# Performance work log

Hardware: AMD Instinct MI355X
Metric: run time of the kernel (lower is better)

Reference implementation:

```python
import jax, jax.numpy as jnp
import numpy as np

VOC = 50257
EMB = 128
N_MEM = 8192
T_Q = 50
T_M = 50
N_HOPS = 3


def setup_inputs() -> dict:
    key = jax.random.key(0)
    ks = jax.random.split(key, 12)
    s = 0.1
    return {
        "query": jax.random.randint(ks[0], (1, T_Q), 0, VOC, dtype=jnp.int32),
        "story": jax.random.randint(ks[1], (N_MEM, T_M), 0, VOC, dtype=jnp.int32),
        "Wa": s * jax.random.normal(ks[2], (VOC, EMB), dtype=jnp.float32),
        "Wc": s * jax.random.normal(ks[3], (VOC, EMB), dtype=jnp.float32),
        "Wb": s * jax.random.normal(ks[4], (VOC, EMB), dtype=jnp.float32),
        "Wt_w": s * jax.random.normal(ks[5], (EMB, EMB), dtype=jnp.float32),
        "Wt_b": jnp.zeros((EMB,), dtype=jnp.float32),
        "H_w": s * jax.random.normal(ks[6], (EMB, EMB), dtype=jnp.float32),
        "H_b": jnp.zeros((EMB,), dtype=jnp.float32),
        "weight_out": s * jax.random.normal(ks[7], (VOC, EMB), dtype=jnp.float32),
        "TA": s * jax.random.normal(ks[8], (N_MEM, EMB), dtype=jnp.float32),
        "TC": s * jax.random.normal(ks[9], (N_MEM, EMB), dtype=jnp.float32),
    }


def reference(query, story, Wa, Wc, Wb, Wt_w, Wt_b, H_w, H_b, weight_out, TA, TC):
    # compute_weights is a stub in the source -> uniform weights 1.0 (plain sum over tokens)
    u = Wb[query].sum(axis=1)                      # [1, E]
    # layer_wise=True: Wa/Wc/Wt shared across hops, so memories are hop-invariant;
    # gather once (same math as recomputing per hop).
    memory_in = Wa[story].sum(axis=1) + TA         # [N, E]
    memory_out = Wc[story].sum(axis=1) + TC        # [N, E]
    for _ in range(N_HOPS):
        attn = jax.nn.softmax(u @ memory_in.T, axis=-1)   # [1, N]
        weighted_out = attn @ memory_out                  # [1, E]
        t = jax.nn.sigmoid(u @ Wt_w.T + Wt_b)             # [1, E]
        u = u * (1.0 - t) + (weighted_out @ H_w.T + H_b) * t
    return jax.nn.log_softmax(u @ weight_out.T, axis=-1)  # [1, V]
```

## Files before the change

kernel.cpp:

```cpp
#include <hip/hip_runtime.h>

#define VOC 50257
#define EMB 128
#define NMEM 8192
#define TQ 50
#define TM 50
#define NHOPS 3

#define MEM_ROWS 4
#define NMEMBLK (NMEM / MEM_ROWS)
#define NHOP 512
#define HROWS (NMEM / NHOP)
#define LOGROWS 64
#define NLOG ((VOC + LOGROWS - 1) / LOGROWS)

#define WS_U      0
#define WS_MIN    (WS_U + EMB)
#define WS_MOUT   (WS_MIN + NMEM*EMB)
#define WS_BSUM   (WS_MOUT + NMEM*EMB)
#define WS_WPART  (WS_BSUM + NHOP)
#define WS_LOGITS (WS_WPART + NHOP*EMB)
#define WS_BPART  (WS_LOGITS + VOC)

__global__ void k_mem_u(const int* __restrict__ story, const int* __restrict__ query,
                        const float* __restrict__ Wa, const float* __restrict__ Wc,
                        const float* __restrict__ Wb, const float* __restrict__ TA,
                        const float* __restrict__ TC, float* __restrict__ min_,
                        float* __restrict__ mout, float* __restrict__ u) {
    int b = blockIdx.x;
    int t = threadIdx.x;
    if (b == NMEMBLK) {
        __shared__ int q[TQ];
        if (t < TQ) q[t] = query[t];
        __syncthreads();
        if (t < EMB) {
            float acc = 0.f;
            for (int i = 0; i < TQ; ++i) acc += Wb[q[i] * EMB + t];
            u[t] = acc;
        }
        return;
    }
    __shared__ int toks[MEM_ROWS * TM];
    if (t < MEM_ROWS * TM) toks[t] = story[b * MEM_ROWS * TM + t];
    __syncthreads();
    int w = t >> 6;
    int lane = t & 63;
    int half = lane >> 5;
    int l = lane & 31;
    int n = b * MEM_ROWS + w;
    float4 a = {0.f, 0.f, 0.f, 0.f};
    float4 c = {0.f, 0.f, 0.f, 0.f};
    #pragma unroll
    for (int tt = 0; tt < TM / 2; ++tt) {
        int tok = toks[w * TM + 2 * tt + half];
        float4 va = ((const float4*)(Wa + tok * EMB))[l];
        float4 vc = ((const float4*)(Wc + tok * EMB))[l];
        a.x += va.x; a.y += va.y; a.z += va.z; a.w += va.w;
        c.x += vc.x; c.y += vc.y; c.z += vc.z; c.w += vc.w;
    }
    a.x += __shfl_xor(a.x, 32); a.y += __shfl_xor(a.y, 32);
    a.z += __shfl_xor(a.z, 32); a.w += __shfl_xor(a.w, 32);
    c.x += __shfl_xor(c.x, 32); c.y += __shfl_xor(c.y, 32);
    c.z += __shfl_xor(c.z, 32); c.w += __shfl_xor(c.w, 32);
    if (half == 0) {
        float4 tv = ((const float4*)(TA + n * EMB))[l];
        a.x += tv.x; a.y += tv.y; a.z += tv.z; a.w += tv.w;
        ((float4*)(min_ + n * EMB))[l] = a;
    } else {
        float4 tv = ((const float4*)(TC + n * EMB))[l];
        c.x += tv.x; c.y += tv.y; c.z += tv.z; c.w += tv.w;
        ((float4*)(mout + n * EMB))[l] = c;
    }
}

__global__ void k_hop(const float* __restrict__ min_, const float* __restrict__ mout,
                      const float* __restrict__ u, float* __restrict__ bsum,
                      float* __restrict__ wpart) {
    int b = blockIdx.x, t = threadIdx.x;
    int w = t >> 6, l = t & 63;
    __shared__ float2 su[64];
    __shared__ float wgt[HROWS];
    __shared__ float part[EMB];
    if (t < 64) su[t] = ((const float2*)u)[t];
    __syncthreads();
    float2 uv = su[l];
    #pragma unroll
    for (int r = 0; r < HROWS / 4; ++r) {
        int rl = w * (HROWS / 4) + r;
        int n = b * HROWS + rl;
        float2 m = ((const float2*)(min_ + n * EMB))[l];
        float p = uv.x * m.x + uv.y * m.y;
        #pragma unroll
        for (int o = 32; o > 0; o >>= 1) p += __shfl_xor(p, o);
        if (l == 0) wgt[rl] = __expf(p);
    }
    __syncthreads();
    if (t < HROWS) {
        float s = wgt[t];
        #pragma unroll
        for (int o = HROWS / 2; o > 0; o >>= 1) s += __shfl_xor(s, o);
        if (t == 0) bsum[b] = s;
    }
    int c = t & 127, h = t >> 7;
    float acc = 0.f;
    #pragma unroll
    for (int r = 0; r < HROWS / 2; ++r) {
        int rl = h * (HROWS / 2) + r;
        acc += wgt[rl] * mout[(b * HROWS + rl) * EMB + c];
    }
    if (h == 0) part[c] = acc;
    __syncthreads();
    if (h == 1) wpart[b * EMB + c] = part[c] + acc;
}

__global__ void k_upd(const float* __restrict__ bsum, const float* __restrict__ wpart,
                      const float* __restrict__ Wt_w, const float* __restrict__ Wt_b,
                      const float* __restrict__ H_w, const float* __restrict__ H_b,
                      float* __restrict__ u) {
    int t = threadIdx.x;
    __shared__ float red[1024];
    __shared__ float wop[8][EMB];
    __shared__ float tga[8][EMB];
    __shared__ float hga[8][EMB];
    __shared__ float us[EMB], wo[EMB];
    __shared__ float gsum_sh;
    red[t] = (t < NHOP) ? bsum[t] : 0.f;
    __syncthreads();
    for (int st = 512; st > 0; st >>= 1) {
        if (t < st) red[t] += red[t + st];
        __syncthreads();
    }
    if (t == 0) gsum_sh = red[0];
    int c = t & 127, h = t >> 7;
    float acc = 0.f;
    for (int r = 0; r < NHOP / 8; ++r) acc += wpart[(h * (NHOP / 8) + r) * EMB + c];
    wop[h][c] = acc;
    if (t < EMB) us[t] = u[t];
    __syncthreads();
    if (t < EMB) {
        float v = 0.f;
        #pragma unroll
        for (int j = 0; j < 8; ++j) v += wop[j][t];
        wo[t] = v / gsum_sh;
    }
    __syncthreads();
    const float4* wt4 = (const float4*)(Wt_w + c * EMB + h * 16);
    const float4* hw4 = (const float4*)(H_w + c * EMB + h * 16);
    float tg = 0.f, hp = 0.f;
    #pragma unroll
    for (int q = 0; q < 4; ++q) {
        float4 wv = wt4[q];
        float4 hv = hw4[q];
        int k0 = h * 16 + q * 4;
        tg += wv.x * us[k0] + wv.y * us[k0 + 1] + wv.z * us[k0 + 2] + wv.w * us[k0 + 3];
        hp += hv.x * wo[k0] + hv.y * wo[k0 + 1] + hv.z * wo[k0 + 2] + hv.w * wo[k0 + 3];
    }
    tga[h][c] = tg;
    hga[h][c] = hp;
    __syncthreads();
    if (t < EMB) {
        float tgs = Wt_b[t], hs = H_b[t];
        #pragma unroll
        for (int j = 0; j < 8; ++j) { tgs += tga[j][t]; hs += hga[j][t]; }
        float gate = 1.f / (1.f + __expf(-tgs));
        u[t] = us[t] * (1.f - gate) + hs * gate;
    }
}

__global__ void k_logits(const float* __restrict__ W, const float* __restrict__ u,
                         float* __restrict__ logits, float* __restrict__ bpart) {
    __shared__ float4 su[32];
    __shared__ float es[8];
    int t = threadIdx.x;
    if (t < 32) su[t] = ((const float4*)u)[t];
    __syncthreads();
    int hw = t >> 5;
    int l2 = t & 31;
    float4 uv = su[l2];
    int v0 = blockIdx.x * LOGROWS + hw * 8;
    float p[8];
    #pragma unroll
    for (int r = 0; r < 8; ++r) {
        int vc = v0 + r; vc = (vc < VOC) ? vc : (VOC - 1);
        float4 wv = ((const float4*)(W + vc * EMB))[l2];
        p[r] = uv.x * wv.x + uv.y * wv.y + uv.z * wv.z + uv.w * wv.w;
    }
    float esum = 0.f;
    #pragma unroll
    for (int r = 0; r < 8; ++r) {
        #pragma unroll
        for (int o = 16; o > 0; o >>= 1) p[r] += __shfl_xor(p[r], o);
        int v = v0 + r;
        if (l2 == 0 && v < VOC) { logits[v] = p[r]; esum += __expf(p[r]); }
    }
    if (l2 == 0) es[hw] = esum;
    __syncthreads();
    if (t == 0) {
        float s = 0.f;
        #pragma unroll
        for (int j = 0; j < 8; ++j) s += es[j];
        bpart[blockIdx.x] = s;
    }
}

__global__ void k_out(const float* __restrict__ logits, const float* __restrict__ bpart,
                      float* __restrict__ out) {
    __shared__ float red[256];
    int t = threadIdx.x;
    float s = 0.f;
    for (int i = t; i < NLOG; i += 256) s += bpart[i];
    red[t] = s; __syncthreads();
    for (int st = 128; st > 0; st >>= 1) {
        if (t < st) red[t] += red[t + st];
        __syncthreads();
    }
    float lse = __logf(red[0]);
    int v = blockIdx.x * 256 + t;
    if (v < VOC) out[v] = logits[v] - lse;
}

extern "C" void kernel_launch(void* const* d_in, const int* in_sizes, int n_in,
                              void* d_out, int out_size, void* d_ws, size_t ws_size,
                              hipStream_t stream) {
    const int*   query = (const int*)d_in[0];
    const int*   story = (const int*)d_in[1];
    const float* Wa    = (const float*)d_in[2];
    const float* Wc    = (const float*)d_in[3];
    const float* Wb    = (const float*)d_in[4];
    const float* Wt_w  = (const float*)d_in[5];
    const float* Wt_b  = (const float*)d_in[6];
    const float* H_w   = (const float*)d_in[7];
    const float* H_b   = (const float*)d_in[8];
    const float* Wout  = (const float*)d_in[9];
    const float* TA    = (const float*)d_in[10];
    const float* TC    = (const float*)d_in[11];
    float* out = (float*)d_out;
    float* ws = (float*)d_ws;

    float* u      = ws + WS_U;
    float* min_   = ws + WS_MIN;
    float* mout   = ws + WS_MOUT;
    float* bsum   = ws + WS_BSUM;
    float* wpart  = ws + WS_WPART;
    float* logits = ws + WS_LOGITS;
    float* bpart  = ws + WS_BPART;

    k_mem_u<<<NMEMBLK + 1, 256, 0, stream>>>(story, query, Wa, Wc, Wb, TA, TC,
                                             min_, mout, u);

    for (int hop = 0; hop < NHOPS; ++hop) {
        k_hop<<<NHOP, 256, 0, stream>>>(min_, mout, u, bsum, wpart);
        k_upd<<<1, 1024, 0, stream>>>(bsum, wpart, Wt_w, Wt_b, H_w, H_b, u);
    }

    k_logits<<<NLOG, 256, 0, stream>>>(Wout, u, logits, bpart);
    k_out<<<(VOC + 255) / 256, 256, 0, stream>>>(logits, bpart, out);
}
```

Measured before the change: 233.2 us.

## Fold per-hop u update into next hop and logits kernels, drop k_upd

Removes the single-block k_upd kernel by having every block of the next hop kernel, and of the logits kernel, redundantly recompute the gated u update from the previous hop's partial sums. Per-hop partials get their own workspace slices so no later kernel overwrites inputs still being read. NHOP drops to 256, so each block handles more memory rows and the redundant reduction over partials is smaller. This saves three launches and their serial gaps, at the cost of every block re-reading the partial sums and the two 128x128 weight matrices, which is duplicated work across hundreds of blocks (notably about 786 logits blocks).

```diff
diff --git a/kernel.cpp b/kernel.cpp
--- a/kernel.cpp
+++ b/kernel.cpp
@@ -9,17 +9,17 @@
 
 #define MEM_ROWS 4
 #define NMEMBLK (NMEM / MEM_ROWS)
-#define NHOP 512
+#define NHOP 256
 #define HROWS (NMEM / NHOP)
 #define LOGROWS 64
 #define NLOG ((VOC + LOGROWS - 1) / LOGROWS)
 
 #define WS_U      0
-#define WS_MIN    (WS_U + EMB)
+#define WS_MIN    (WS_U + 4*EMB)
 #define WS_MOUT   (WS_MIN + NMEM*EMB)
 #define WS_BSUM   (WS_MOUT + NMEM*EMB)
-#define WS_WPART  (WS_BSUM + NHOP)
-#define WS_LOGITS (WS_WPART + NHOP*EMB)
+#define WS_WPART  (WS_BSUM + 3*NHOP)
+#define WS_LOGITS (WS_WPART + 3*NHOP*EMB)
 #define WS_BPART  (WS_LOGITS + VOC)
 
 __global__ void k_mem_u(const int* __restrict__ story, const int* __restrict__ query,
@@ -73,22 +73,94 @@
     }
 }
 
-__global__ void k_hop(const float* __restrict__ min_, const float* __restrict__ mout,
-                      const float* __restrict__ u, float* __restrict__ bsum,
-                      float* __restrict__ wpart) {
-    int b = blockIdx.x, t = threadIdx.x;
-    int w = t >> 6, l = t & 63;
-    __shared__ float2 su[64];
+__device__ __forceinline__ void finalize_u(const float* __restrict__ bsumP,
+                                           const float* __restrict__ wpartP,
+                                           const float* __restrict__ u_prev,
+                                           const float* __restrict__ Wt_w,
+                                           const float* __restrict__ Wt_b,
+                                           const float* __restrict__ H_w,
+                                           const float* __restrict__ H_b,
+                                           float* __restrict__ u_out,
+                                           float* unew ) {
+    __shared__ float red[NHOP];
+    __shared__ float wop[2][EMB];
+    __shared__ float tga[2][EMB], hga[2][EMB];
+    __shared__ float us[EMB], wo[EMB];
+    __shared__ float gsum_sh;
+    int t = threadIdx.x;
+    red[t] = bsumP[t];
+    __syncthreads();
+    for (int st = 128; st > 0; st >>= 1) {
+        if (t < st) red[t] += red[t + st];
+        __syncthreads();
+    }
+    if (t == 0) gsum_sh = red[0];
+    int e = t & 127, h = t >> 7;
+    float acc = 0.f;
+    for (int j = 0; j < NHOP / 2; ++j) acc += wpartP[(h * (NHOP / 2) + j) * EMB + e];
+    wop[h][e] = acc;
+    if (t < EMB) us[t] = u_prev[t];
+    __syncthreads();
+    if (t < EMB) wo[t] = (wop[0][t] + wop[1][t]) / gsum_sh;
+    __syncthreads();
+    const float4* wt4 = (const float4*)(Wt_w + e * EMB + h * 64);
+    const float4* hw4 = (const float4*)(H_w + e * EMB + h * 64);
+    float tg = 0.f, hp = 0.f;
+    #pragma unroll
+    for (int q = 0; q < 16; ++q) {
+        float4 wv = wt4[q];
+        float4 hv = hw4[q];
+        int k0 = h * 64 + q * 4;
+        tg += wv.x * us[k0] + wv.y * us[k0 + 1] + wv.z * us[k0 + 2] + wv.w * us[k0 + 3];
+        hp += hv.x * wo[k0] + hv.y * wo[k0 + 1] + hv.z * wo[k0 + 2] + hv.w * wo[k0 + 3];
+    }
+    tga[h][e] = tg;
+    hga[h][e] = hp;
+    __syncthreads();
+    if (t < EMB) {
+        float tgs = Wt_b[t] + tga[0][t] + tga[1][t];
+        float hs  = H_b[t]  + hga[0][t] + hga[1][t];
+        float gate = 1.f / (1.f + __expf(-tgs));
+        float un = us[t] * (1.f - gate) + hs * gate;
+        unew[t] = un;
+        if (u_out) u_out[t] = un;
+    }
+    __syncthreads();
+}
+
+template <int H>
+__global__ __launch_bounds__(256) void k_hop(const float* __restrict__ min_,
+                                             const float* __restrict__ mout,
+                                             float* __restrict__ uarr,
+                                             const float* __restrict__ Wt_w,
+                                             const float* __restrict__ Wt_b,
+                                             const float* __restrict__ H_w,
+                                             const float* __restrict__ H_b,
+                                             float* __restrict__ bsum_all,
+                                             float* __restrict__ wpart_all) {
+    __shared__ float unew[EMB];
+    __shared__ float2 su2[64];
     __shared__ float wgt[HROWS];
     __shared__ float part[EMB];
-    if (t < 64) su[t] = ((const float2*)u)[t];
-    __syncthreads();
-    float2 uv = su[l];
+    int b = blockIdx.x, t = threadIdx.x;
+    if (H > 0) {
+        finalize_u(bsum_all + (H - 1) * NHOP, wpart_all + (H - 1) * NHOP * EMB,
+                   uarr + (H - 1) * EMB, Wt_w, Wt_b, H_w, H_b,
+                   uarr + H * EMB, unew);
+        if (t < 64) su2[t] = ((const float2*)unew)[t];
+    } else {
+        if (t < 64) su2[t] = ((const float2*)uarr)[t];
+    }
+    __syncthreads();
+    float* bsum = bsum_all + H * NHOP;
+    float* wpart = wpart_all + H * NHOP * EMB;
+    int w = t >> 6, l = t & 63;
+    float2 uv = su2[l];
+    int n0 = b * HROWS;
     #pragma unroll
     for (int r = 0; r < HROWS / 4; ++r) {
         int rl = w * (HROWS / 4) + r;
-        int n = b * HROWS + rl;
-        float2 m = ((const float2*)(min_ + n * EMB))[l];
+        float2 m = ((const float2*)(min_ + (n0 + rl) * EMB))[l];
         float p = uv.x * m.x + uv.y * m.y;
         #pragma unroll
         for (int o = 32; o > 0; o >>= 1) p += __shfl_xor(p, o);
@@ -106,77 +178,31 @@
     #pragma unroll
     for (int r = 0; r < HROWS / 2; ++r) {
         int rl = h * (HROWS / 2) + r;
-        acc += wgt[rl] * mout[(b * HROWS + rl) * EMB + c];
+        acc += wgt[rl] * mout[(n0 + rl) * EMB + c];
     }
     if (h == 0) part[c] = acc;
     __syncthreads();
     if (h == 1) wpart[b * EMB + c] = part[c] + acc;
 }
 
-__global__ void k_upd(const float* __restrict__ bsum, const float* __restrict__ wpart,
-                      const float* __restrict__ Wt_w, const float* __restrict__ Wt_b,
-                      const float* __restrict__ H_w, const float* __restrict__ H_b,
-                      float* __restrict__ u) {
-    int t = threadIdx.x;
-    __shared__ float red[1024];
-    __shared__ float wop[8][EMB];
-    __shared__ float tga[8][EMB];
-    __shared__ float hga[8][EMB];
-    __shared__ float us[EMB], wo[EMB];
-    __shared__ float gsum_sh;
-    red[t] = (t < NHOP) ? bsum[t] : 0.f;
-    __syncthreads();
-    for (int st = 512; st > 0; st >>= 1) {
-        if (t < st) red[t] += red[t + st];
-        __syncthreads();
-    }
-    if (t == 0) gsum_sh = red[0];
-    int c = t & 127, h = t >> 7;
-    float acc = 0.f;
-    for (int r = 0; r < NHOP / 8; ++r) acc += wpart[(h * (NHOP / 8) + r) * EMB + c];
-    wop[h][c] = acc;
-    if (t < EMB) us[t] = u[t];
-    __syncthreads();
-    if (t < EMB) {
-        float v = 0.f;
-        #pragma unroll
-        for (int j = 0; j < 8; ++j) v += wop[j][t];
-        wo[t] = v / gsum_sh;
-    }
-    __syncthreads();
-    const float4* wt4 = (const float4*)(Wt_w + c * EMB + h * 16);
-    const float4* hw4 = (const float4*)(H_w + c * EMB + h * 16);
-    float tg = 0.f, hp = 0.f;
-    #pragma unroll
-    for (int q = 0; q < 4; ++q) {
-        float4 wv = wt4[q];
-        float4 hv = hw4[q];
-        int k0 = h * 16 + q * 4;
-        tg += wv.x * us[k0] + wv.y * us[k0 + 1] + wv.z * us[k0 + 2] + wv.w * us[k0 + 3];
-        hp += hv.x * wo[k0] + hv.y * wo[k0 + 1] + hv.z * wo[k0 + 2] + hv.w * wo[k0 + 3];
-    }
-    tga[h][c] = tg;
-    hga[h][c] = hp;
-    __syncthreads();
-    if (t < EMB) {
-        float tgs = Wt_b[t], hs = H_b[t];
-        #pragma unroll
-        for (int j = 0; j < 8; ++j) { tgs += tga[j][t]; hs += hga[j][t]; }
-        float gate = 1.f / (1.f + __expf(-tgs));
-        u[t] = us[t] * (1.f - gate) + hs * gate;
-    }
-}
-
-__global__ void k_logits(const float* __restrict__ W, const float* __restrict__ u,
-                         float* __restrict__ logits, float* __restrict__ bpart) {
-    __shared__ float4 su[32];
+__global__ __launch_bounds__(256) void k_logits(const float* __restrict__ W,
+                                                float* __restrict__ uarr,
+                                                const float* __restrict__ Wt_w,
+                                                const float* __restrict__ Wt_b,
+                                                const float* __restrict__ H_w,
+                                                const float* __restrict__ H_b,
+                                                const float* __restrict__ bsum_all,
+                                                const float* __restrict__ wpart_all,
+                                                float* __restrict__ logits,
+                                                float* __restrict__ bpart) {
+    __shared__ float unew[EMB];
     __shared__ float es[8];
     int t = threadIdx.x;
-    if (t < 32) su[t] = ((const float4*)u)[t];
-    __syncthreads();
+    finalize_u(bsum_all + 2 * NHOP, wpart_all + 2 * NHOP * EMB,
+               uarr + 2 * EMB, Wt_w, Wt_b, H_w, H_b, nullptr, unew);
     int hw = t >> 5;
     int l2 = t & 31;
-    float4 uv = su[l2];
+    float4 uv = ((const float4*)unew)[l2];
     int v0 = blockIdx.x * LOGROWS + hw * 8;
     float p[8];
     #pragma unroll
@@ -237,7 +263,7 @@
     float* out = (float*)d_out;
     float* ws = (float*)d_ws;
 
-    float* u      = ws + WS_U;
+    float* uarr   = ws + WS_U;
     float* min_   = ws + WS_MIN;
     float* mout   = ws + WS_MOUT;
     float* bsum   = ws + WS_BSUM;
@@ -246,13 +272,14 @@
     float* bpart  = ws + WS_BPART;
 
     k_mem_u<<<NMEMBLK + 1, 256, 0, stream>>>(story, query, Wa, Wc, Wb, TA, TC,
-                                             min_, mout, u);
-
-    for (int hop = 0; hop < NHOPS; ++hop) {
-        k_hop<<<NHOP, 256, 0, stream>>>(min_, mout, u, bsum, wpart);
-        k_upd<<<1, 1024, 0, stream>>>(bsum, wpart, Wt_w, Wt_b, H_w, H_b, u);
-    }
-
-    k_logits<<<NLOG, 256, 0, stream>>>(Wout, u, logits, bpart);
+                                             min_, mout, uarr);
+    k_hop<0><<<NHOP, 256, 0, stream>>>(min_, mout, uarr, Wt_w, Wt_b, H_w, H_b,
+                                       bsum, wpart);
+    k_hop<1><<<NHOP, 256, 0, stream>>>(min_, mout, uarr, Wt_w, Wt_b, H_w, H_b,
+                                       bsum, wpart);
+    k_hop<2><<<NHOP, 256, 0, stream>>>(min_, mout, uarr, Wt_w, Wt_b, H_w, H_b,
+                                       bsum, wpart);
+    k_logits<<<NLOG, 256, 0, stream>>>(Wout, uarr, Wt_w, Wt_b, H_w, H_b,
+                                       bsum, wpart, logits, bpart);
     k_out<<<(VOC + 255) / 256, 256, 0, stream>>>(logits, bpart, out);
 }
```

Result: slower. 329.4 us (+41.2%).
